# Kernel optimization log

Measured on AMD Instinct MI355X. Metric: run time of the kernel, lower is better.

The kernel has to match this reference:

```python
import jax, jax.numpy as jnp
import numpy as np

EPS = 1e-5
N_HEAD = 8

def setup_inputs() -> dict:
    key = jax.random.key(0)
    ks = jax.random.split(key, 8)
    n, c, h, w = 8, 512, 64, 64
    feats_in = 512
    x = jax.random.normal(ks[0], (n, c, h, w), jnp.float32)
    cond = jax.random.normal(ks[1], (n, feats_in), jnp.float32)
    # AdaGN linear: feats_in -> 2*c
    W_ada = jax.random.normal(ks[2], (feats_in, 2 * c), jnp.float32) * (1.0 / np.sqrt(feats_in))
    b_ada = jnp.zeros((2 * c,), jnp.float32)
    # qkv 1x1 conv: c -> 3c
    W_qkv = jax.random.normal(ks[3], (3 * c, c), jnp.float32) * (1.0 / np.sqrt(c))
    b_qkv = jnp.zeros((3 * c,), jnp.float32)
    # out 1x1 conv: c -> c
    W_out = jax.random.normal(ks[4], (c, c), jnp.float32) * (1.0 / np.sqrt(c))
    b_out = jnp.zeros((c,), jnp.float32)
    return {"x": x, "cond": cond, "W_ada": W_ada, "b_ada": b_ada,
            "W_qkv": W_qkv, "b_qkv": b_qkv, "W_out": W_out, "b_out": b_out}

def reference(x, cond, W_ada, b_ada, W_qkv, b_qkv, W_out, b_out):
    n, c, h, w = x.shape
    nh = N_HEAD
    dh = c // nh
    s = h * w
    # AdaGN: GroupNorm with 1 group, no affine, then scale/shift from cond
    scales_shifts = cond @ W_ada + b_ada  # [n, 2c]
    scales, shifts = scales_shifts[:, :c], scales_shifts[:, c:]
    xf = x.reshape(n, -1)
    mean = xf.mean(axis=1, keepdims=True)
    var = xf.var(axis=1, keepdims=True)
    normed = ((xf - mean) * jax.lax.rsqrt(var + EPS)).reshape(n, c, h, w)
    normed = shifts[:, :, None, None] + normed * (scales[:, :, None, None] + 1.0)
    # qkv 1x1 conv
    qkv = jnp.einsum('nchw,oc->nohw', normed, W_qkv) + b_qkv[None, :, None, None]
    # view [n, nh*3, dh, s] then transpose -> [n, nh*3, s, dh]
    qkv = qkv.reshape(n, nh * 3, dh, s).transpose(0, 1, 3, 2)
    q, k, v = jnp.split(qkv, 3, axis=1)  # each [n, nh, s, dh]
    scale = dh ** (-0.25)
    att = jnp.einsum('nhsd,nhtd->nhst', q * scale, k * scale)
    att = jax.nn.softmax(att, axis=-1)
    y = jnp.einsum('nhst,nhtd->nhsd', att, v)  # [n, nh, s, dh]
    y = y.transpose(0, 1, 3, 2).reshape(n, c, h, w)
    out = jnp.einsum('nchw,oc->nohw', y, W_out) + b_out[None, :, None, None]
    return x + out
```

## Files before the change

kernel.cpp:

```cpp
#include <hip/hip_runtime.h>

#define NB   8
#define CC   512
#define SS   4096
#define NHD  8
#define DH   64
#define FEAT 512
#define NPER (CC*SS)

typedef unsigned short ushort_t;
typedef __attribute__((ext_vector_type(8))) short bf16x8;
typedef __attribute__((ext_vector_type(4))) float f32x4;

__device__ inline float b2f(ushort_t h) {
    union { unsigned int u; float f; } v; v.u = ((unsigned int)h) << 16; return v.f;
}
__device__ inline ushort_t f2b(float f) {
    union { float f; unsigned int u; } v; v.f = f;
    unsigned int u = v.u;
    u += 0x7fffu + ((u >> 16) & 1u);
    return (ushort_t)(u >> 16);
}
__device__ inline void unpack8(uint4 v, ushort_t* us) {
    us[0] = v.x & 0xffff; us[1] = v.x >> 16;
    us[2] = v.y & 0xffff; us[3] = v.y >> 16;
    us[4] = v.z & 0xffff; us[5] = v.z >> 16;
    us[6] = v.w & 0xffff; us[7] = v.w >> 16;
}
__device__ inline float loadIn(const void* p, size_t idx, int isf) {
    return isf ? ((const float*)p)[idx] : b2f(((const ushort_t*)p)[idx]);
}
__device__ inline void load8(const void* p, size_t idx, int isf, float* f) {
    if (isf) {
        const float* q = (const float*)p + idx;
        float4 a = *(const float4*)q, b = *(const float4*)(q + 4);
        f[0]=a.x; f[1]=a.y; f[2]=a.z; f[3]=a.w; f[4]=b.x; f[5]=b.y; f[6]=b.z; f[7]=b.w;
    } else {
        uint4 v = *(const uint4*)((const ushort_t*)p + idx);
        ushort_t us[8]; unpack8(v, us);
        for (int j = 0; j < 8; ++j) f[j] = b2f(us[j]);
    }
}

typedef __attribute__((address_space(1))) const unsigned int gas_u32;
typedef __attribute__((address_space(3))) unsigned int las_u32;
__device__ inline void gload_lds16(const void* g, void* l) {
    __builtin_amdgcn_global_load_lds((gas_u32*)g, (las_u32*)l, 16, 0, 0);
}

__global__ void probe_kernel(const unsigned int* __restrict__ x, int* __restrict__ flag) {
    unsigned int w = x[threadIdx.x & 63];
    unsigned int elo = (w >> 7) & 0xFF;
    int hit = (elo >= 0x60 && elo <= 0x9F) ? 1 : 0;
    for (int m = 1; m < 64; m <<= 1) hit += __shfl_xor(hit, m, 64);
    if (threadIdx.x == 0) *flag = (hit >= 40) ? 0 : 1;
}

__global__ __launch_bounds__(256) void ada_kernel(
    const void* __restrict__ cond, const void* __restrict__ W,
    const void* __restrict__ bias, float* __restrict__ out,
    const int* __restrict__ flagp)
{
    int isf = *flagp;
    int n = blockIdx.x;
    int j = blockIdx.y * 256 + threadIdx.x;
    float acc = loadIn(bias, j, isf);
    for (int k = 0; k < FEAT; ++k)
        acc += loadIn(cond, (size_t)n * FEAT + k, isf) * loadIn(W, (size_t)k * (2 * CC) + j, isf);
    out[n * (2 * CC) + j] = acc;
}

__global__ __launch_bounds__(256) void stats_kernel(
    const void* __restrict__ x, float* __restrict__ part, const int* __restrict__ flagp)
{
    int isf = *flagp;
    int n = blockIdx.x, blk = blockIdx.y;
    int tid = threadIdx.x;
    float s = 0.f, ss = 0.f;
    size_t base8 = (size_t)blk * 4096 + tid;
    for (int i = 0; i < 16; ++i) {
        float f[8];
        load8(x, ((size_t)n * NPER) + (base8 + (size_t)i * 256) * 8, isf, f);
        for (int j = 0; j < 8; ++j) { s += f[j]; ss += f[j] * f[j]; }
    }
    for (int m = 1; m < 64; m <<= 1) { s += __shfl_xor(s, m, 64); ss += __shfl_xor(ss, m, 64); }
    int w = tid >> 6;
    if ((tid & 63) == 0) {
        part[(size_t)n * 512 + (blk * 4 + w) * 2 + 0] = s;
        part[(size_t)n * 512 + (blk * 4 + w) * 2 + 1] = ss;
    }
}

__global__ __launch_bounds__(256) void coef_kernel(
    const float* __restrict__ ada, const float* __restrict__ part,
    float* __restrict__ coefA, float* __restrict__ coefB)
{
    __shared__ float reds[4], redss[4], mv[2];
    int n = blockIdx.x;
    int tid = threadIdx.x;
    float s  = part[(size_t)n * 512 + tid * 2 + 0];
    float ss = part[(size_t)n * 512 + tid * 2 + 1];
    for (int m = 1; m < 64; m <<= 1) { s += __shfl_xor(s, m, 64); ss += __shfl_xor(ss, m, 64); }
    int w = tid >> 6, lane = tid & 63;
    if (lane == 0) { reds[w] = s; redss[w] = ss; }
    __syncthreads();
    if (tid == 0) {
        float S  = (reds[0] + reds[1]) + (reds[2] + reds[3]);
        float S2 = (redss[0] + redss[1]) + (redss[2] + redss[3]);
        float inv = 1.f / (float)NPER;
        float mean = S * inv;
        float var  = S2 * inv - mean * mean;
        mv[0] = mean;
        mv[1] = rsqrtf(var + 1e-5f);
    }
    __syncthreads();
    float mean = mv[0], r = mv[1];
    int c = blockIdx.y * 256 + tid;
    float a = (ada[n * (2 * CC) + c] + 1.f) * r;
    coefA[n * CC + c] = a;
    coefB[n * CC + c] = ada[n * (2 * CC) + CC + c] - mean * a;
}

__global__ __launch_bounds__(256) void wprime_kernel(
    const void* __restrict__ W, const void* __restrict__ bias,
    const float* __restrict__ coefA, const float* __restrict__ coefB,
    ushort_t* __restrict__ Wp, float* __restrict__ bias2,
    const int* __restrict__ flagp)
{
    int isf = *flagp;
    int n = blockIdx.x;
    int o = blockIdx.y * 256 + threadIdx.x;
    const float* cA = coefA + n * CC;
    const float* cB = coefB + n * CC;
    float bacc = loadIn(bias, o, isf);
    ushort_t* dst = Wp + ((size_t)n * 1536 + o) * 512;
    for (int c = 0; c < 512; c += 8) {
        float wv[8];
        load8(W, (size_t)o * 512 + c, isf, wv);
        float4 a0 = *(const float4*)&cA[c], a1 = *(const float4*)&cA[c + 4];
        float4 b0 = *(const float4*)&cB[c], b1 = *(const float4*)&cB[c + 4];
        float av[8] = {a0.x, a0.y, a0.z, a0.w, a1.x, a1.y, a1.z, a1.w};
        float bv[8] = {b0.x, b0.y, b0.z, b0.w, b1.x, b1.y, b1.z, b1.w};
        ushort_t pk[8];
        for (int j = 0; j < 8; ++j) {
            bacc += wv[j] * bv[j];
            pk[j] = f2b(wv[j] * av[j]);
        }
        *(ushort4*)&dst[c]     = make_ushort4(pk[0], pk[1], pk[2], pk[3]);
        *(ushort4*)&dst[c + 4] = make_ushort4(pk[4], pk[5], pk[6], pk[7]);
    }
    bias2[n * 1536 + o] = bacc;
}

__global__ __launch_bounds__(256) void wconv_kernel(
    const void* __restrict__ W, ushort_t* __restrict__ Wb, const int* __restrict__ flagp)
{
    int isf = *flagp;
    size_t i = ((size_t)blockIdx.x * 256 + threadIdx.x) * 8;
    float f[8];
    load8(W, i, isf, f);
    ushort_t pk[8];
    for (int j = 0; j < 8; ++j) pk[j] = f2b(f[j]);
    *(ushort4*)&Wb[i]     = make_ushort4(pk[0], pk[1], pk[2], pk[3]);
    *(ushort4*)&Wb[i + 4] = make_ushort4(pk[4], pk[5], pk[6], pk[7]);
}

__global__ __launch_bounds__(256) void qkv_gemm_kernel(
    const ushort_t* __restrict__ Wp, const void* __restrict__ X,
    const float* __restrict__ bias2, ushort_t* __restrict__ C,
    const int* __restrict__ flagp, int nb, int hb, int hc)
{
    __shared__ __align__(16) short Alds[64][64];
    __shared__ __align__(16) short Blds[64][72];
    int isf = *flagp;
    int z = blockIdx.z;
    int nIdx = nb + z;
    int yb = blockIdx.y;
    int p = yb / hc, hh = yb % hc;
    int arow0 = p * 512 + (hb + hh) * 64;
    size_t cbase = ((size_t)(z * 3 + p) * (hc * 64) + hh * 64) * SS;
    int n0 = blockIdx.x * 64;
    int tid = threadIdx.x;
    int w = tid >> 6, lane = tid & 63;
    int quad = lane >> 4, l16 = lane & 15;
    int wm = (w >> 1) * 32, wn = (w & 1) * 32;
    const ushort_t* Arow = Wp + ((size_t)nIdx * 1536 + arow0) * 512;
    f32x4 acc[2][2] = {};

    for (int k0 = 0; k0 < 512; k0 += 64) {
        __syncthreads();
        for (int it = 0; it < 2; ++it) {
            int chunk = it * 256 + tid;
            int row = chunk >> 3;
            int ssl = (chunk & 7) ^ (row & 7);
            int cb0 = it * 256 + w * 64;
            gload_lds16(&Arow[(size_t)row * 512 + k0 + ssl * 8], (short*)Alds + cb0 * 8);
        }
        for (int it = 0; it < 2; ++it) {
            int chunk = tid + it * 256;
            int cc = chunk >> 3, hb8 = chunk & 7;
            int ch = k0 + cc;
            float f[8];
            load8(X, (size_t)nIdx * NPER + (size_t)ch * SS + n0 + hb8 * 8, isf, f);
            for (int j = 0; j < 8; ++j)
                Blds[hb8 * 8 + j][cc] = (short)f2b(f[j]);
        }
        __syncthreads();
        for (int kk = 0; kk < 2; ++kk) {
            bf16x8 af[2], bfv[2];
            for (int mi = 0; mi < 2; ++mi)
                af[mi] = *(const bf16x8*)&Alds[wm + mi * 16 + l16]
                                              [((kk * 4 + quad) ^ (l16 & 7)) * 8];
            for (int ni = 0; ni < 2; ++ni)
                bfv[ni] = *(const bf16x8*)&Blds[wn + ni * 16 + l16][kk * 32 + quad * 8];
            for (int mi = 0; mi < 2; ++mi)
                for (int ni = 0; ni < 2; ++ni)
                    acc[mi][ni] = __builtin_amdgcn_mfma_f32_16x16x32_bf16(
                        af[mi], bfv[ni], acc[mi][ni], 0, 0, 0);
        }
    }
    const float* b2p = bias2 + (size_t)nIdx * 1536;
    if (p < 2) {
        const float SCL = 0.42467078f;
        for (int mi = 0; mi < 2; ++mi)
            for (int ni = 0; ni < 2; ++ni) {
                int col = n0 + wn + ni * 16 + l16;
                int d0 = wm + mi * 16 + quad * 4;
                ushort_t pk[4];
                for (int r = 0; r < 4; ++r) {
                    float v = (acc[mi][ni][r] + b2p[arow0 + d0 + r]) * SCL;
                    pk[r] = f2b(v);
                }
                *(ushort4*)&C[cbase + (size_t)col * 64 + d0] =
                    make_ushort4(pk[0], pk[1], pk[2], pk[3]);
            }
    } else {
        for (int mi = 0; mi < 2; ++mi)
            for (int ni = 0; ni < 2; ++ni) {
                int col = n0 + wn + ni * 16 + l16;
                for (int r = 0; r < 4; ++r) {
                    int rowl = wm + mi * 16 + quad * 4 + r;
                    float v = acc[mi][ni][r] + b2p[arow0 + rowl];
                    C[cbase + (size_t)rowl * SS + col] = f2b(v);
                }
            }
    }
}

__global__ __launch_bounds__(256, 4) void attn_kernel(
    const ushort_t* __restrict__ qkv,
    ushort_t* __restrict__ y,
    int nb, int hb, int hc)
{
    __shared__ __align__(16) short Klds[2][64][64];
    __shared__ __align__(16) short Vlds[2][64][64];

    int s0 = blockIdx.x * 128;
    int hl = blockIdx.y;
    int z = blockIdx.z;
    int n = nb + z;
    int hcc = hc * 64;
    const ushort_t* Q = qkv + ((size_t)(z * 3 + 0) * hcc + hl * 64) * SS;
    const ushort_t* K = qkv + ((size_t)(z * 3 + 1) * hcc + hl * 64) * SS;
    const ushort_t* V = qkv + ((size_t)(z * 3 + 2) * hcc + hl * 64) * SS;

    int tid = threadIdx.x;
    int w = tid >> 6, lane = tid & 63;
    int quad = lane >> 4, l16 = lane & 15;
    int sw = l16 & 7;

    bf16x8 qf[2][2];
    for (int si = 0; si < 2; ++si)
        for (int kk = 0; kk < 2; ++kk)
            qf[si][kk] = *(const bf16x8*)&Q[(size_t)(s0 + w * 32 + si * 16 + l16) * 64
                                            + kk * 32 + quad * 8];

    auto stage = [&](int b, int tt) {
        #pragma unroll
        for (int it = 0; it < 2; ++it) {
            int chunk = it * 256 + tid;
            int row = chunk >> 3;
            int ssl = (chunk & 7) ^ (row & 7);
            int cb0 = it * 256 + w * 64;
            gload_lds16(&K[(size_t)(tt + row) * 64 + ssl * 8], (short*)Klds[b] + cb0 * 8);
            gload_lds16(&V[(size_t)row * SS + tt + ssl * 8],   (short*)Vlds[b] + cb0 * 8);
        }
    };

    const short ONE = 0x3F80;
    bf16x8 ones = { ONE, ONE, ONE, ONE, ONE, ONE, ONE, ONE };

    f32x4 o[2][4] = {};
    f32x4 sum_acc[2] = {};

    stage(0, 0);

    for (int t0 = 0; t0 < SS; t0 += 64) {
        int cur = (t0 >> 6) & 1;
        __syncthreads();
        if (t0 + 64 < SS) stage(cur ^ 1, t0 + 64);

        for (int kk = 0; kk < 2; ++kk) {
            f32x4 sv[2][2];
            for (int ntl = 0; ntl < 2; ++ntl) {
                int nt = kk * 2 + ntl;
                bf16x8 kf0 = *(const bf16x8*)&Klds[cur][nt * 16 + l16][((0 * 4 + quad) ^ sw) * 8];
                bf16x8 kf1 = *(const bf16x8*)&Klds[cur][nt * 16 + l16][((1 * 4 + quad) ^ sw) * 8];
                for (int si = 0; si < 2; ++si) {
                    f32x4 a = { -16.f, -16.f, -16.f, -16.f };
                    a = __builtin_amdgcn_mfma_f32_16x16x32_bf16(kf0, qf[si][0], a, 0, 0, 0);
                    a = __builtin_amdgcn_mfma_f32_16x16x32_bf16(kf1, qf[si][1], a, 0, 0, 0);
                    sv[ntl][si] = a;
                }
            }

            bf16x8 vf[4];
            for (int dt = 0; dt < 4; ++dt)
                vf[dt] = *(const bf16x8*)&Vlds[cur][dt * 16 + l16][((kk * 4 + quad) ^ sw) * 8];

            for (int si = 0; si < 2; ++si) {
                float p0 = exp2f(sv[0][si][0]), p1 = exp2f(sv[0][si][1]);
                float p2 = exp2f(sv[0][si][2]), p3 = exp2f(sv[0][si][3]);
                float p4 = exp2f(sv[1][si][0]), p5 = exp2f(sv[1][si][1]);
                float p6 = exp2f(sv[1][si][2]), p7 = exp2f(sv[1][si][3]);
                unsigned int x0, x1, y0, y1;
                asm("v_cvt_pk_bf16_f32 %0, %1, %2" : "=v"(x0) : "v"(p0), "v"(p1));
                asm("v_cvt_pk_bf16_f32 %0, %1, %2" : "=v"(x1) : "v"(p2), "v"(p3));
                asm("v_cvt_pk_bf16_f32 %0, %1, %2" : "=v"(y0) : "v"(p4), "v"(p5));
                asm("v_cvt_pk_bf16_f32 %0, %1, %2" : "=v"(y1) : "v"(p6), "v"(p7));
                asm("v_permlane32_swap_b32 %0, %1" : "+v"(x0), "+v"(y0));
                asm("v_permlane32_swap_b32 %0, %1" : "+v"(x1), "+v"(y1));
                asm("v_permlane16_swap_b32 %0, %1" : "+v"(x0), "+v"(y0));
                asm("v_permlane16_swap_b32 %0, %1" : "+v"(x1), "+v"(y1));
                union { unsigned int u[4]; bf16x8 v; } frag;
                frag.u[0] = x0; frag.u[1] = x1; frag.u[2] = y0; frag.u[3] = y1;

                sum_acc[si] = __builtin_amdgcn_mfma_f32_16x16x32_bf16(frag.v, ones, sum_acc[si], 0, 0, 0);
                for (int dt = 0; dt < 4; ++dt)
                    o[si][dt] = __builtin_amdgcn_mfma_f32_16x16x32_bf16(frag.v, vf[dt], o[si][dt], 0, 0, 0);
            }
        }
    }

    for (int si = 0; si < 2; ++si) {
        f32x4 inv;
        for (int r = 0; r < 4; ++r) inv[r] = 1.0f / sum_acc[si][r];
        for (int dt = 0; dt < 4; ++dt) {
            int d = dt * 16 + l16;
            int cidx = (hb + hl) * DH + d;
            size_t bidx = ((size_t)n * CC + cidx) * SS + s0 + w * 32 + si * 16 + quad * 4;
            ushort_t pk[4];
            for (int r = 0; r < 4; ++r) pk[r] = f2b(o[si][dt][r] * inv[r]);
            *(ushort4*)&y[bidx] = make_ushort4(pk[0], pk[1], pk[2], pk[3]);
        }
    }
}

__global__ __launch_bounds__(512) void out_gemm_kernel(
    const ushort_t* __restrict__ Wb, const void* __restrict__ bias, const void* __restrict__ x,
    const ushort_t* __restrict__ ybuf, float* __restrict__ out,
    const int* __restrict__ flagp)
{
    __shared__ __align__(16) short Ylds[64][264];
    int isf = *flagp;
    int n = blockIdx.y;
    int s0 = blockIdx.x * 64;
    int tid = threadIdx.x;
    int w = tid >> 6, lane = tid & 63;
    int quad = lane >> 4, l16 = lane & 15;
    const ushort_t* Yb = ybuf + (size_t)n * ((size_t)CC * SS);
    float* Op = out + (size_t)n * NPER;

    f32x4 acc[4][4] = {};
    for (int kh = 0; kh < 2; ++kh) {
        __syncthreads();
        int ch = (tid & 255) + kh * 256;
        int cg = tid >> 8;
        for (int cb = 0; cb < 4; ++cb) {
            uint4 v = *(const uint4*)&Yb[(size_t)ch * SS + s0 + cg * 32 + cb * 8];
            ushort_t us[8]; unpack8(v, us);
            for (int j = 0; j < 8; ++j) Ylds[cg * 32 + cb * 8 + j][tid & 255] = (short)us[j];
        }
        __syncthreads();
        for (int k0 = 0; k0 < 256; k0 += 32) {
            bf16x8 af[4];
            for (int mi = 0; mi < 4; ++mi)
                af[mi] = *(const bf16x8*)&Wb[(size_t)(w * 64 + mi * 16 + l16) * 512
                                             + kh * 256 + k0 + quad * 8];
            for (int ni = 0; ni < 4; ++ni) {
                bf16x8 bfv = *(const bf16x8*)&Ylds[ni * 16 + l16][k0 + quad * 8];
                for (int mi = 0; mi < 4; ++mi)
                    acc[mi][ni] = __builtin_amdgcn_mfma_f32_16x16x32_bf16(
                        af[mi], bfv, acc[mi][ni], 0, 0, 0);
            }
        }
    }

    for (int mi = 0; mi < 4; ++mi)
        for (int ni = 0; ni < 4; ++ni) {
            int col = s0 + ni * 16 + l16;
            for (int r = 0; r < 4; ++r) {
                int m = w * 64 + mi * 16 + quad * 4 + r;
                size_t idx = (size_t)m * SS + col;
                float v = acc[mi][ni][r] + loadIn(bias, m, isf)
                        + loadIn(x, (size_t)n * NPER + idx, isf);
                Op[idx] = v;
            }
        }
}

extern "C" void kernel_launch(void* const* d_in, const int* in_sizes, int n_in,
                              void* d_out, int out_size, void* d_ws, size_t ws_size,
                              hipStream_t stream) {
    (void)in_sizes; (void)n_in; (void)out_size;
    const void* x     = d_in[0];
    const void* cond  = d_in[1];
    const void* W_ada = d_in[2];
    const void* b_ada = d_in[3];
    const void* W_qkv = d_in[4];
    const void* b_qkv = d_in[5];
    const void* W_out = d_in[6];
    const void* b_out = d_in[7];
    float* out = (float*)d_out;

    char* ws = (char*)d_ws;
    float* part   = (float*)ws;
    float* ada    = (float*)(ws + 16384);
    float* coefA  = (float*)(ws + 49152);
    float* coefB  = (float*)(ws + 65536);
    int*   flag   = (int*)(ws + 81920);
    ushort_t* woutb  = (ushort_t*)(ws + 82176);
    float* bias2  = (float*)(ws + 606464);
    ushort_t* wprime = (ushort_t*)(ws + 655616);
    ushort_t* ybuf   = (ushort_t*)(ws + 13238528);
    const size_t BASE = 13238528ULL + (size_t)NB * NPER * 2;
    ushort_t* qkvbuf = (ushort_t*)(ws + BASE);

    const size_t PER_HS = (size_t)3 * 64 * SS * 2;
    size_t avail = ws_size > BASE ? ws_size - BASE : 0;
    int NC = 1, HC = 1;
    if      (avail >= 64 * PER_HS) { NC = 8; HC = 8; }
    else if (avail >= 32 * PER_HS) { NC = 4; HC = 8; }
    else if (avail >= 16 * PER_HS) { NC = 2; HC = 8; }
    else if (avail >=  8 * PER_HS) { NC = 1; HC = 8; }
    else if (avail >=  4 * PER_HS) { NC = 1; HC = 4; }
    else if (avail >=  2 * PER_HS) { NC = 1; HC = 2; }

    probe_kernel <<<1, 64, 0, stream>>>((const unsigned int*)x, flag);
    ada_kernel   <<<dim3(NB, 4),  256, 0, stream>>>(cond, W_ada, b_ada, ada, flag);
    stats_kernel <<<dim3(NB, 64), 256, 0, stream>>>(x, part, flag);
    coef_kernel  <<<dim3(NB, 2),  256, 0, stream>>>(ada, part, coefA, coefB);
    wprime_kernel<<<dim3(NB, 6),  256, 0, stream>>>(W_qkv, b_qkv, coefA, coefB, wprime, bias2, flag);
    wconv_kernel <<<dim3(128),    256, 0, stream>>>(W_out, woutb, flag);

    for (int nb = 0; nb < NB; nb += NC)
        for (int hb = 0; hb < NHD; hb += HC) {
            qkv_gemm_kernel<<<dim3(64, 3 * HC, NC), 256, 0, stream>>>(
                wprime, x, bias2, qkvbuf, flag, nb, hb, HC);
            attn_kernel<<<dim3(32, HC, NC), 256, 0, stream>>>(
                qkvbuf, ybuf, nb, hb, HC);
        }

    out_gemm_kernel<<<dim3(64, NB), 512, 0, stream>>>(woutb, b_out, x, ybuf, out, flag);
}
```

Measured before the change: 909.4 us.

## Pre-transpose x to bf16 and compute all three QKV projections per block

Adds a kernel that converts x to bf16 once and stores it transposed as [n, s, c], so the QKV GEMM can stream its B tile with direct global-to-LDS loads instead of converting fp32 and scatter-writing into LDS on every k step. The QKV GEMM now computes Q, K and V for one head in the same block, so each B tile is reused across three A tiles instead of being reloaded three times. It also reorders the grid so the batch index is the fastest-varying dimension. In exchange it adds a 32 MB workspace buffer and an extra full pass over x, triples the accumulator registers, and moves the qkv buffer offset, which leaves less workspace for chunking.

```diff
diff --git a/kernel.cpp b/kernel.cpp
--- a/kernel.cpp
+++ b/kernel.cpp
@@ -165,85 +165,123 @@
     *(ushort4*)&Wb[i + 4] = make_ushort4(pk[4], pk[5], pk[6], pk[7]);
 }
 
+__global__ __launch_bounds__(256) void xt_kernel(
+    const void* __restrict__ x, ushort_t* __restrict__ xt, const int* __restrict__ flagp)
+{
+    __shared__ __align__(16) short xl[64][72];
+    int isf = *flagp;
+    int st = blockIdx.x & 63, ct = blockIdx.x >> 6;
+    int n = blockIdx.y;
+    int s0 = st * 64, c0 = ct * 64;
+    int tid = threadIdx.x;
+    for (int it = 0; it < 2; ++it) {
+        int t = tid + it * 256;
+        int cr = t >> 3, sc8 = t & 7;
+        float f[8];
+        load8(x, ((size_t)n * CC + c0 + cr) * SS + s0 + sc8 * 8, isf, f);
+        ushort_t pk[8];
+        for (int j = 0; j < 8; ++j) pk[j] = f2b(f[j]);
+        *(ushort4*)&xl[cr][sc8 * 8]     = make_ushort4(pk[0], pk[1], pk[2], pk[3]);
+        *(ushort4*)&xl[cr][sc8 * 8 + 4] = make_ushort4(pk[4], pk[5], pk[6], pk[7]);
+    }
+    __syncthreads();
+    for (int it = 0; it < 2; ++it) {
+        int t = tid + it * 256;
+        int sr = t >> 3, cc8 = t & 7;
+        ushort_t pk[8];
+        for (int j = 0; j < 8; ++j) pk[j] = (ushort_t)xl[cc8 * 8 + j][sr];
+        size_t o = ((size_t)n * SS + s0 + sr) * CC + c0 + cc8 * 8;
+        *(ushort4*)&xt[o]     = make_ushort4(pk[0], pk[1], pk[2], pk[3]);
+        *(ushort4*)&xt[o + 4] = make_ushort4(pk[4], pk[5], pk[6], pk[7]);
+    }
+}
+
 __global__ __launch_bounds__(256) void qkv_gemm_kernel(
-    const ushort_t* __restrict__ Wp, const void* __restrict__ X,
+    const ushort_t* __restrict__ Wp, const ushort_t* __restrict__ xt,
     const float* __restrict__ bias2, ushort_t* __restrict__ C,
-    const int* __restrict__ flagp, int nb, int hb, int hc)
-{
-    __shared__ __align__(16) short Alds[64][64];
-    __shared__ __align__(16) short Blds[64][72];
-    int isf = *flagp;
-    int z = blockIdx.z;
+    int nb, int hb, int hc)
+{
+    __shared__ __align__(16) short Alds[3][64][64];
+    __shared__ __align__(16) short Blds[64][64];
+    int z = blockIdx.x;
     int nIdx = nb + z;
-    int yb = blockIdx.y;
-    int p = yb / hc, hh = yb % hc;
-    int arow0 = p * 512 + (hb + hh) * 64;
-    size_t cbase = ((size_t)(z * 3 + p) * (hc * 64) + hh * 64) * SS;
-    int n0 = blockIdx.x * 64;
+    int n0 = blockIdx.y * 64;
+    int hh = blockIdx.z;
+    int head = hb + hh;
+    int hcc = hc * 64;
     int tid = threadIdx.x;
     int w = tid >> 6, lane = tid & 63;
     int quad = lane >> 4, l16 = lane & 15;
     int wm = (w >> 1) * 32, wn = (w & 1) * 32;
-    const ushort_t* Arow = Wp + ((size_t)nIdx * 1536 + arow0) * 512;
-    f32x4 acc[2][2] = {};
+    const ushort_t* Ab = Wp + ((size_t)nIdx * 1536 + head * 64) * 512;
+    const ushort_t* Bb = xt + ((size_t)nIdx * SS + n0) * 512;
+    f32x4 acc[3][2][2] = {};
+
+    int chunk0 = tid, chunk1 = tid + 256;
+    int row0 = chunk0 >> 3, ssl0 = (chunk0 & 7) ^ (row0 & 7);
+    int row1 = chunk1 >> 3, ssl1 = (chunk1 & 7) ^ (row1 & 7);
+    int cb0a = w * 64, cb0b = 256 + w * 64;
 
     for (int k0 = 0; k0 < 512; k0 += 64) {
         __syncthreads();
-        for (int it = 0; it < 2; ++it) {
-            int chunk = it * 256 + tid;
-            int row = chunk >> 3;
-            int ssl = (chunk & 7) ^ (row & 7);
-            int cb0 = it * 256 + w * 64;
-            gload_lds16(&Arow[(size_t)row * 512 + k0 + ssl * 8], (short*)Alds + cb0 * 8);
-        }
-        for (int it = 0; it < 2; ++it) {
-            int chunk = tid + it * 256;
-            int cc = chunk >> 3, hb8 = chunk & 7;
-            int ch = k0 + cc;
-            float f[8];
-            load8(X, (size_t)nIdx * NPER + (size_t)ch * SS + n0 + hb8 * 8, isf, f);
-            for (int j = 0; j < 8; ++j)
-                Blds[hb8 * 8 + j][cc] = (short)f2b(f[j]);
+        gload_lds16(&Bb[(size_t)row0 * 512 + k0 + ssl0 * 8], (short*)Blds + cb0a * 8);
+        gload_lds16(&Bb[(size_t)row1 * 512 + k0 + ssl1 * 8], (short*)Blds + cb0b * 8);
+        #pragma unroll
+        for (int p = 0; p < 3; ++p) {
+            const ushort_t* Ap = Ab + (size_t)p * 512 * 512;
+            gload_lds16(&Ap[(size_t)row0 * 512 + k0 + ssl0 * 8], (short*)Alds[p] + cb0a * 8);
+            gload_lds16(&Ap[(size_t)row1 * 512 + k0 + ssl1 * 8], (short*)Alds[p] + cb0b * 8);
         }
         __syncthreads();
         for (int kk = 0; kk < 2; ++kk) {
-            bf16x8 af[2], bfv[2];
+            bf16x8 bfv[2];
+            for (int ni = 0; ni < 2; ++ni)
+                bfv[ni] = *(const bf16x8*)&Blds[wn + ni * 16 + l16]
+                                               [((kk * 4 + quad) ^ (l16 & 7)) * 8];
+            #pragma unroll
+            for (int p = 0; p < 3; ++p) {
+                bf16x8 af[2];
+                for (int mi = 0; mi < 2; ++mi)
+                    af[mi] = *(const bf16x8*)&Alds[p][wm + mi * 16 + l16]
+                                                     [((kk * 4 + quad) ^ (l16 & 7)) * 8];
+                for (int mi = 0; mi < 2; ++mi)
+                    for (int ni = 0; ni < 2; ++ni)
+                        acc[p][mi][ni] = __builtin_amdgcn_mfma_f32_16x16x32_bf16(
+                            af[mi], bfv[ni], acc[p][mi][ni], 0, 0, 0);
+            }
+        }
+    }
+
+    const float* b2p = bias2 + (size_t)nIdx * 1536;
+    #pragma unroll
+    for (int p = 0; p < 3; ++p) {
+        int arow0 = p * 512 + head * 64;
+        size_t cbase = ((size_t)(z * 3 + p) * hcc + hh * 64) * SS;
+        if (p < 2) {
+            const float SCL = 0.42467078f;
             for (int mi = 0; mi < 2; ++mi)
-                af[mi] = *(const bf16x8*)&Alds[wm + mi * 16 + l16]
-                                              [((kk * 4 + quad) ^ (l16 & 7)) * 8];
-            for (int ni = 0; ni < 2; ++ni)
-                bfv[ni] = *(const bf16x8*)&Blds[wn + ni * 16 + l16][kk * 32 + quad * 8];
+                for (int ni = 0; ni < 2; ++ni) {
+                    int col = n0 + wn + ni * 16 + l16;
+                    int d0 = wm + mi * 16 + quad * 4;
+                    ushort_t pk[4];
+                    for (int r = 0; r < 4; ++r) {
+                        float v = (acc[p][mi][ni][r] + b2p[arow0 + d0 + r]) * SCL;
+                        pk[r] = f2b(v);
+                    }
+                    *(ushort4*)&C[cbase + (size_t)col * 64 + d0] =
+                        make_ushort4(pk[0], pk[1], pk[2], pk[3]);
+                }
+        } else {
             for (int mi = 0; mi < 2; ++mi)
-                for (int ni = 0; ni < 2; ++ni)
-                    acc[mi][ni] = __builtin_amdgcn_mfma_f32_16x16x32_bf16(
-                        af[mi], bfv[ni], acc[mi][ni], 0, 0, 0);
-        }
-    }
-    const float* b2p = bias2 + (size_t)nIdx * 1536;
-    if (p < 2) {
-        const float SCL = 0.42467078f;
-        for (int mi = 0; mi < 2; ++mi)
-            for (int ni = 0; ni < 2; ++ni) {
-                int col = n0 + wn + ni * 16 + l16;
-                int d0 = wm + mi * 16 + quad * 4;
-                ushort_t pk[4];
-                for (int r = 0; r < 4; ++r) {
-                    float v = (acc[mi][ni][r] + b2p[arow0 + d0 + r]) * SCL;
-                    pk[r] = f2b(v);
+                for (int ni = 0; ni < 2; ++ni) {
+                    int col = n0 + wn + ni * 16 + l16;
+                    for (int r = 0; r < 4; ++r) {
+                        int rowl = wm + mi * 16 + quad * 4 + r;
+                        float v = acc[p][mi][ni][r] + b2p[arow0 + rowl];
+                        C[cbase + (size_t)rowl * SS + col] = f2b(v);
+                    }
                 }
-                *(ushort4*)&C[cbase + (size_t)col * 64 + d0] =
-                    make_ushort4(pk[0], pk[1], pk[2], pk[3]);
-            }
-    } else {
-        for (int mi = 0; mi < 2; ++mi)
-            for (int ni = 0; ni < 2; ++ni) {
-                int col = n0 + wn + ni * 16 + l16;
-                for (int r = 0; r < 4; ++r) {
-                    int rowl = wm + mi * 16 + quad * 4 + r;
-                    float v = acc[mi][ni][r] + b2p[arow0 + rowl];
-                    C[cbase + (size_t)rowl * SS + col] = f2b(v);
-                }
-            }
+        }
     }
 }
 
@@ -433,7 +471,8 @@
     float* bias2  = (float*)(ws + 606464);
     ushort_t* wprime = (ushort_t*)(ws + 655616);
     ushort_t* ybuf   = (ushort_t*)(ws + 13238528);
-    const size_t BASE = 13238528ULL + (size_t)NB * NPER * 2;
+    ushort_t* xtb    = (ushort_t*)(ws + 46792960);
+    const size_t BASE = 46792960ULL + 33554432ULL;
     ushort_t* qkvbuf = (ushort_t*)(ws + BASE);
 
     const size_t PER_HS = (size_t)3 * 64 * SS * 2;
@@ -452,11 +491,12 @@
     coef_kernel  <<<dim3(NB, 2),  256, 0, stream>>>(ada, part, coefA, coefB);
     wprime_kernel<<<dim3(NB, 6),  256, 0, stream>>>(W_qkv, b_qkv, coefA, coefB, wprime, bias2, flag);
     wconv_kernel <<<dim3(128),    256, 0, stream>>>(W_out, woutb, flag);
+    xt_kernel    <<<dim3(512, NB), 256, 0, stream>>>(x, xtb, flag);
 
     for (int nb = 0; nb < NB; nb += NC)
         for (int hb = 0; hb < NHD; hb += HC) {
-            qkv_gemm_kernel<<<dim3(64, 3 * HC, NC), 256, 0, stream>>>(
-                wprime, x, bias2, qkvbuf, flag, nb, hb, HC);
+            qkv_gemm_kernel<<<dim3(NC, 64, HC), 256, 0, stream>>>(
+                wprime, xtb, bias2, qkvbuf, nb, hb, HC);
             attn_kernel<<<dim3(32, HC, NC), 256, 0, stream>>>(
                 qkvbuf, ybuf, nb, hb, HC);
         }
```

Measured after the change: 841.4 us. 1.08x faster.
